# Optimization experiments

Measured on AMD Instinct MI355X. Metric: run time of the kernel, lower is better.

The kernel has to match this reference:

```python
import jax, jax.numpy as jnp
import numpy as np

N = 100000
NNZ = 3200000
F = 128


def setup_inputs() -> dict:
    key = jax.random.key(0)
    k1, k2, k3 = jax.random.split(key, 3)
    x = jax.random.normal(k1, (N, F), dtype=jnp.float32)
    A_ind = jax.random.randint(k2, (2, NNZ), 0, N, dtype=jnp.int64)
    A_val = jax.random.normal(k3, (NNZ,), dtype=jnp.float32)
    return {"x": x, "A_ind": A_ind, "A_val": A_val}


def reference(x, A_ind, A_val):
    # COO SpMM: out[r] = sum over edges e with row[e]==r of A_val[e] * x[col[e]]
    # coalesce() in torch sums duplicate (row, col) entries; segment_sum over
    # rows yields identical math without explicit sorting/deduplication.
    row, col = A_ind[0], A_ind[1]
    contrib = A_val[:, None] * x[col]            # [nnz, F] gather + scale
    out = jax.ops.segment_sum(contrib, row, num_segments=x.shape[0])  # scatter-add
    return out
```

## Files before the change

### kernel.cpp

```cpp
#include <hip/hip_runtime.h>

#define F 128
#define RPB 64
#define MAXNB 1792
#define CHUNK 8192
#define EPT 32
#define CAP 3072
#define SPMM_T 512
#define HELD (CAP/SPMM_T)

__global__ void spmm_coo_atomic(const int* __restrict__ rows,
                                const int* __restrict__ cols,
                                const float* __restrict__ vals,
                                const float* __restrict__ x,
                                float* __restrict__ out,
                                int nnz, int n_rows) {
    int t = blockIdx.x * blockDim.x + threadIdx.x;
    int e = t >> 5;
    int g = t & 31;
    if (e >= nnz) return;
    int r = rows[e];
    int c = cols[e];
    float v = vals[e];
    if ((unsigned)r >= (unsigned)n_rows || (unsigned)c >= (unsigned)n_rows) return;
    const float4 xv = *reinterpret_cast<const float4*>(x + (size_t)c * F + g * 4);
    float* o = out + (size_t)r * F + g * 4;
    atomicAdd(o + 0, v * xv.x);
    atomicAdd(o + 1, v * xv.y);
    atomicAdd(o + 2, v * xv.z);
    atomicAdd(o + 3, v * xv.w);
}

__device__ __forceinline__ unsigned f2bf(float f) {
    unsigned u = __float_as_uint(f);
    return (u + 0x7FFFu + ((u >> 16) & 1u)) >> 16;
}

__global__ void k_cvt_bf16(const float* __restrict__ x, unsigned short* __restrict__ xb,
                           long long total) {
    long long i = ((long long)blockIdx.x * 256 + threadIdx.x) * 8;
    if (i >= total) return;
    float4 a = *reinterpret_cast<const float4*>(x + i);
    float4 b = *reinterpret_cast<const float4*>(x + i + 4);
    uint4 o;
    o.x = f2bf(a.x) | (f2bf(a.y) << 16);
    o.y = f2bf(a.z) | (f2bf(a.w) << 16);
    o.z = f2bf(b.x) | (f2bf(b.y) << 16);
    o.w = f2bf(b.z) | (f2bf(b.w) << 16);
    *reinterpret_cast<uint4*>(xb + i) = o;
}

__global__ void k_bucket_histo(const int* __restrict__ rows, int* __restrict__ cnt,
                               int nnz, int nbk, int n) {
    __shared__ int lc[MAXNB];
    for (int i = threadIdx.x; i < nbk; i += 256) lc[i] = 0;
    __syncthreads();
    int base = blockIdx.x * CHUNK;
#pragma unroll
    for (int k = 0; k < EPT; ++k) {
        int e = base + k * 256 + threadIdx.x;
        if (e < nnz) {
            int r = rows[e];
            if ((unsigned)r < (unsigned)n) atomicAdd(&lc[r / RPB], 1);
        }
    }
    __syncthreads();
    for (int i = threadIdx.x; i < nbk; i += 256) {
        int c = lc[i];
        if (c) atomicAdd(&cnt[i], c);
    }
}

__global__ void k_bucket_scan(const int* __restrict__ cnt, int* __restrict__ off,
                              int* __restrict__ gcur, int nbk) {
    __shared__ int s[256];
    int tid = threadIdx.x;
    int per = (nbk + 255) / 256;
    int base = tid * per;
    int loc[8];
    int tsum = 0;
#pragma unroll
    for (int k = 0; k < 8; ++k) {
        int i = base + k;
        int v = (k < per && i < nbk) ? cnt[i] : 0;
        loc[k] = v;
        tsum += v;
    }
    s[tid] = tsum;
    __syncthreads();
    for (int o = 1; o < 256; o <<= 1) {
        int t = (tid >= o) ? s[tid - o] : 0;
        __syncthreads();
        s[tid] += t;
        __syncthreads();
    }
    int run = s[tid] - tsum;
#pragma unroll
    for (int k = 0; k < 8; ++k) {
        int i = base + k;
        if (k < per && i < nbk) { off[i] = run; gcur[i] = run; }
        run += loc[k];
    }
    if (tid == 255) off[nbk] = s[255];
}

__global__ void k_rank_scatter(const int* __restrict__ rows, const int* __restrict__ cols,
                               const float* __restrict__ vals, int* __restrict__ gcur,
                               int2* __restrict__ pair, int nnz, int nbk, int n) {
    __shared__ int lcnt[MAXNB];
    __shared__ int lbase[MAXNB];
    for (int i = threadIdx.x; i < nbk; i += 256) lcnt[i] = 0;
    __syncthreads();
    int base = blockIdx.x * CHUNK;
    unsigned br[EPT];
#pragma unroll
    for (int k = 0; k < EPT; ++k) {
        int e = base + k * 256 + threadIdx.x;
        br[k] = 0xFFFFFFFFu;
        if (e < nnz) {
            int r = rows[e];
            if ((unsigned)r < (unsigned)n) {
                int b = r / RPB;
                int rk = atomicAdd(&lcnt[b], 1);
                br[k] = ((unsigned)b << 13) | (unsigned)rk;
            }
        }
    }
    __syncthreads();
    for (int i = threadIdx.x; i < nbk; i += 256) {
        int c = lcnt[i];
        if (c) lbase[i] = atomicAdd(&gcur[i], c);
    }
    __syncthreads();
#pragma unroll
    for (int k = 0; k < EPT; ++k) {
        if (br[k] != 0xFFFFFFFFu) {
            int e = base + k * 256 + threadIdx.x;
            int b = br[k] >> 13;
            int rk = br[k] & 0x1FFF;
            int lr = rows[e] - b * RPB;
            int c = cols[e];
            if ((unsigned)c >= (unsigned)n) c = 0;
            int pos = lbase[b] + rk;
            pair[pos] = make_int2((lr << 17) | c, __float_as_int(vals[e]));
        }
    }
}

__global__ void __launch_bounds__(SPMM_T) k_sort_spmm(const int* __restrict__ off,
                                                      const int2* __restrict__ pair,
                                                      const unsigned short* __restrict__ xb,
                                                      float* __restrict__ out, int n) {
    __shared__ int2 eb[CAP];
    __shared__ int rcnt[RPB];
    __shared__ int rst[RPB + 1];
    __shared__ int rcur[RPB];

    int b = blockIdx.x;
    int tid = threadIdx.x;
    int wave = tid >> 6;
    int lane = tid & 63;
    int q = lane >> 4;
    int fl = lane & 15;

    int beg = off[b], end = off[b + 1];
    bool first = true;
    int bb = beg;
    do {
        int bn = min(CAP, end - bb);
        if (tid < RPB) rcnt[tid] = 0;
        __syncthreads();

        int2 held[HELD];
#pragma unroll
        for (int k = 0; k < HELD; ++k) {
            int j = tid + k * SPMM_T;
            held[k] = make_int2(0, 0);
            if (j < bn) {
                int2 pr = pair[bb + j];
                held[k] = pr;
                atomicAdd(&rcnt[pr.x >> 17], 1);
            }
        }
        __syncthreads();

        if (tid < 64) {
            int v = rcnt[tid];
            int s = v;
            for (int o = 1; o < 64; o <<= 1) {
                int t = __shfl_up(s, o);
                if (tid >= o) s += t;
            }
            rst[tid + 1] = s;
            if (tid == 0) rst[0] = 0;
            rcur[tid] = s - v;
        }
        __syncthreads();

#pragma unroll
        for (int k = 0; k < HELD; ++k) {
            int j = tid + k * SPMM_T;
            if (j < bn) {
                int2 pr = held[k];
                int lr = pr.x >> 17;
                int pos = atomicAdd(&rcur[lr], 1);
                eb[pos] = make_int2(pr.x & 0x1FFFF, pr.y);
            }
        }
        __syncthreads();

        for (int rr = 0; rr < 8; ++rr) {
            int lr = wave * 8 + rr;
            int s0 = rst[lr], s1 = rst[lr + 1];
            float acc[8] = {0.f, 0.f, 0.f, 0.f, 0.f, 0.f, 0.f, 0.f};
#pragma unroll 2
            for (int j = s0 + q; j < s1; j += 4) {
                int2 e = eb[j];
                int col = e.x;
                float vk = __int_as_float(e.y);
                uint4 w = *reinterpret_cast<const uint4*>(xb + (size_t)col * F + fl * 8);
                acc[0] += vk * __uint_as_float(w.x << 16);
                acc[1] += vk * __uint_as_float(w.x & 0xFFFF0000u);
                acc[2] += vk * __uint_as_float(w.y << 16);
                acc[3] += vk * __uint_as_float(w.y & 0xFFFF0000u);
                acc[4] += vk * __uint_as_float(w.z << 16);
                acc[5] += vk * __uint_as_float(w.z & 0xFFFF0000u);
                acc[6] += vk * __uint_as_float(w.w << 16);
                acc[7] += vk * __uint_as_float(w.w & 0xFFFF0000u);
            }
#pragma unroll
            for (int i = 0; i < 8; ++i) {
                acc[i] += __shfl_xor(acc[i], 16);
                acc[i] += __shfl_xor(acc[i], 32);
            }
            if (q == 0) {
                long long row = (long long)b * RPB + lr;
                if (row < n) {
                    float* po = out + (size_t)row * F + fl * 8;
                    float4 lo = make_float4(acc[0], acc[1], acc[2], acc[3]);
                    float4 hi = make_float4(acc[4], acc[5], acc[6], acc[7]);
                    if (first) {
                        *reinterpret_cast<float4*>(po) = lo;
                        *reinterpret_cast<float4*>(po + 4) = hi;
                    } else {
                        float4 t0 = *reinterpret_cast<const float4*>(po);
                        float4 t1 = *reinterpret_cast<const float4*>(po + 4);
                        t0.x += lo.x; t0.y += lo.y; t0.z += lo.z; t0.w += lo.w;
                        t1.x += hi.x; t1.y += hi.y; t1.z += hi.z; t1.w += hi.w;
                        *reinterpret_cast<float4*>(po) = t0;
                        *reinterpret_cast<float4*>(po + 4) = t1;
                    }
                }
            }
        }
        first = false;
        bb += CAP;
        __syncthreads();
    } while (bb < end);
}

extern "C" void kernel_launch(void* const* d_in, const int* in_sizes, int n_in,
                              void* d_out, int out_size, void* d_ws, size_t ws_size,
                              hipStream_t stream) {
    const float* x = (const float*)d_in[0];
    const int* A_ind = (const int*)d_in[1];
    const float* A_val = (const float*)d_in[2];
    float* out = (float*)d_out;

    const int nnz = in_sizes[2];
    const int n = out_size / F;
    const int nbk = (n + RPB - 1) / RPB;
    const int* rows = A_ind;
    const int* cols = A_ind + nnz;

    const long long xtotal = (long long)n * F;

    const size_t need = (size_t)nnz * 8
                      + (size_t)xtotal * 2
                      + (size_t)(3 * nbk + 1) * 4 + 128;

    if (nbk > MAXNB || (xtotal % 8) != 0 || ws_size < need) {
        hipMemsetAsync(d_out, 0, (size_t)out_size * sizeof(float), stream);
        const long long total = (long long)nnz * 32;
        spmm_coo_atomic<<<(int)((total + 255) / 256), 256, 0, stream>>>(
            rows, cols, A_val, x, out, nnz, n);
        return;
    }

    char* w = (char*)d_ws;
    int2* pair = (int2*)w;            w += (size_t)nnz * 8;
    unsigned short* xb = (unsigned short*)w;  w += (size_t)xtotal * 2;
    int* cnt = (int*)w;               w += (size_t)nbk * 4;
    int* off = (int*)w;               w += (size_t)(nbk + 1) * 4;
    int* gcur = (int*)w;

    const int nchunks = (nnz + CHUNK - 1) / CHUNK;

    k_cvt_bf16<<<(int)(xtotal / 8 + 255) / 256, 256, 0, stream>>>(x, xb, xtotal);
    hipMemsetAsync(cnt, 0, (size_t)nbk * 4, stream);
    k_bucket_histo<<<nchunks, 256, 0, stream>>>(rows, cnt, nnz, nbk, n);
    k_bucket_scan<<<1, 256, 0, stream>>>(cnt, off, gcur, nbk);
    k_rank_scatter<<<nchunks, 256, 0, stream>>>(rows, cols, A_val, gcur, pair,
                                                nnz, nbk, n);
    k_sort_spmm<<<nbk, SPMM_T, 0, stream>>>(off, pair, xb, out, n);
}
```

Baseline: 223.5 us.

## Fuse bf16 conversion with histogram and make SpMM kernel persistent

Merges the x-to-bf16 conversion kernel and the bucket histogram kernel into a single launch, splitting blocks by index, so one launch is saved and the two independent jobs can overlap. The sort-SpMM kernel becomes a grid-stride persistent kernel capped at 1024 blocks instead of one block per bucket. With ~1563 buckets, some blocks now process two buckets serially, which may cause load imbalance at the tail.

```diff
diff --git a/kernel.cpp b/kernel.cpp
--- a/kernel.cpp
+++ b/kernel.cpp
@@ -8,6 +8,7 @@
 #define CAP 3072
 #define SPMM_T 512
 #define HELD (CAP/SPMM_T)
+#define PERSIST 1024
 
 __global__ void spmm_coo_atomic(const int* __restrict__ rows,
                                 const int* __restrict__ cols,
@@ -36,38 +37,39 @@
     return (u + 0x7FFFu + ((u >> 16) & 1u)) >> 16;
 }
 
-__global__ void k_cvt_bf16(const float* __restrict__ x, unsigned short* __restrict__ xb,
-                           long long total) {
-    long long i = ((long long)blockIdx.x * 256 + threadIdx.x) * 8;
-    if (i >= total) return;
-    float4 a = *reinterpret_cast<const float4*>(x + i);
-    float4 b = *reinterpret_cast<const float4*>(x + i + 4);
-    uint4 o;
-    o.x = f2bf(a.x) | (f2bf(a.y) << 16);
-    o.y = f2bf(a.z) | (f2bf(a.w) << 16);
-    o.z = f2bf(b.x) | (f2bf(b.y) << 16);
-    o.w = f2bf(b.z) | (f2bf(b.w) << 16);
-    *reinterpret_cast<uint4*>(xb + i) = o;
-}
-
-__global__ void k_bucket_histo(const int* __restrict__ rows, int* __restrict__ cnt,
-                               int nnz, int nbk, int n) {
+__global__ void k_cvt_histo(const float* __restrict__ x, unsigned short* __restrict__ xb,
+                            long long xtotal,
+                            const int* __restrict__ rows, int* __restrict__ cnt,
+                            int nnz, int nbk, int n, int cvtb) {
     __shared__ int lc[MAXNB];
-    for (int i = threadIdx.x; i < nbk; i += 256) lc[i] = 0;
-    __syncthreads();
-    int base = blockIdx.x * CHUNK;
-#pragma unroll
-    for (int k = 0; k < EPT; ++k) {
-        int e = base + k * 256 + threadIdx.x;
-        if (e < nnz) {
-            int r = rows[e];
-            if ((unsigned)r < (unsigned)n) atomicAdd(&lc[r / RPB], 1);
+    if ((int)blockIdx.x < cvtb) {
+        long long i = ((long long)blockIdx.x * 256 + threadIdx.x) * 8;
+        if (i >= xtotal) return;
+        float4 a = *reinterpret_cast<const float4*>(x + i);
+        float4 b = *reinterpret_cast<const float4*>(x + i + 4);
+        uint4 o;
+        o.x = f2bf(a.x) | (f2bf(a.y) << 16);
+        o.y = f2bf(a.z) | (f2bf(a.w) << 16);
+        o.z = f2bf(b.x) | (f2bf(b.y) << 16);
+        o.w = f2bf(b.z) | (f2bf(b.w) << 16);
+        *reinterpret_cast<uint4*>(xb + i) = o;
+    } else {
+        for (int i = threadIdx.x; i < nbk; i += 256) lc[i] = 0;
+        __syncthreads();
+        int base = ((int)blockIdx.x - cvtb) * CHUNK;
+#pragma unroll
+        for (int k = 0; k < EPT; ++k) {
+            int e = base + k * 256 + threadIdx.x;
+            if (e < nnz) {
+                int r = rows[e];
+                if ((unsigned)r < (unsigned)n) atomicAdd(&lc[r / RPB], 1);
+            }
         }
-    }
-    __syncthreads();
-    for (int i = threadIdx.x; i < nbk; i += 256) {
-        int c = lc[i];
-        if (c) atomicAdd(&cnt[i], c);
+        __syncthreads();
+        for (int i = threadIdx.x; i < nbk; i += 256) {
+            int c = lc[i];
+            if (c) atomicAdd(&cnt[i], c);
+        }
     }
 }
 
@@ -150,113 +152,115 @@
 __global__ void __launch_bounds__(SPMM_T) k_sort_spmm(const int* __restrict__ off,
                                                       const int2* __restrict__ pair,
                                                       const unsigned short* __restrict__ xb,
-                                                      float* __restrict__ out, int n) {
+                                                      float* __restrict__ out,
+                                                      int n, int nbk) {
     __shared__ int2 eb[CAP];
     __shared__ int rcnt[RPB];
     __shared__ int rst[RPB + 1];
     __shared__ int rcur[RPB];
 
-    int b = blockIdx.x;
     int tid = threadIdx.x;
     int wave = tid >> 6;
     int lane = tid & 63;
     int q = lane >> 4;
     int fl = lane & 15;
 
-    int beg = off[b], end = off[b + 1];
-    bool first = true;
-    int bb = beg;
-    do {
-        int bn = min(CAP, end - bb);
-        if (tid < RPB) rcnt[tid] = 0;
-        __syncthreads();
-
-        int2 held[HELD];
-#pragma unroll
-        for (int k = 0; k < HELD; ++k) {
-            int j = tid + k * SPMM_T;
-            held[k] = make_int2(0, 0);
-            if (j < bn) {
-                int2 pr = pair[bb + j];
-                held[k] = pr;
-                atomicAdd(&rcnt[pr.x >> 17], 1);
-            }
-        }
-        __syncthreads();
-
-        if (tid < 64) {
-            int v = rcnt[tid];
-            int s = v;
-            for (int o = 1; o < 64; o <<= 1) {
-                int t = __shfl_up(s, o);
-                if (tid >= o) s += t;
-            }
-            rst[tid + 1] = s;
-            if (tid == 0) rst[0] = 0;
-            rcur[tid] = s - v;
-        }
-        __syncthreads();
-
-#pragma unroll
-        for (int k = 0; k < HELD; ++k) {
-            int j = tid + k * SPMM_T;
-            if (j < bn) {
-                int2 pr = held[k];
-                int lr = pr.x >> 17;
-                int pos = atomicAdd(&rcur[lr], 1);
-                eb[pos] = make_int2(pr.x & 0x1FFFF, pr.y);
-            }
-        }
-        __syncthreads();
-
-        for (int rr = 0; rr < 8; ++rr) {
-            int lr = wave * 8 + rr;
-            int s0 = rst[lr], s1 = rst[lr + 1];
-            float acc[8] = {0.f, 0.f, 0.f, 0.f, 0.f, 0.f, 0.f, 0.f};
+    for (int b = blockIdx.x; b < nbk; b += gridDim.x) {
+        int beg = off[b], end = off[b + 1];
+        bool first = true;
+        int bb = beg;
+        do {
+            int bn = min(CAP, end - bb);
+            if (tid < RPB) rcnt[tid] = 0;
+            __syncthreads();
+
+            int2 held[HELD];
+#pragma unroll
+            for (int k = 0; k < HELD; ++k) {
+                int j = tid + k * SPMM_T;
+                held[k] = make_int2(0, 0);
+                if (j < bn) {
+                    int2 pr = pair[bb + j];
+                    held[k] = pr;
+                    atomicAdd(&rcnt[pr.x >> 17], 1);
+                }
+            }
+            __syncthreads();
+
+            if (tid < RPB) {
+                int v = rcnt[tid];
+                int s = v;
+                for (int o = 1; o < RPB; o <<= 1) {
+                    int t = __shfl_up(s, o);
+                    if (tid >= o) s += t;
+                }
+                rst[tid + 1] = s;
+                if (tid == 0) rst[0] = 0;
+                rcur[tid] = s - v;
+            }
+            __syncthreads();
+
+#pragma unroll
+            for (int k = 0; k < HELD; ++k) {
+                int j = tid + k * SPMM_T;
+                if (j < bn) {
+                    int2 pr = held[k];
+                    int lr = pr.x >> 17;
+                    int pos = atomicAdd(&rcur[lr], 1);
+                    eb[pos] = make_int2(pr.x & 0x1FFFF, pr.y);
+                }
+            }
+            __syncthreads();
+
+            for (int rr = 0; rr < 8; ++rr) {
+                int lr = wave * 8 + rr;
+                int s0 = rst[lr], s1 = rst[lr + 1];
+                float acc[8] = {0.f, 0.f, 0.f, 0.f, 0.f, 0.f, 0.f, 0.f};
 #pragma unroll 2
-            for (int j = s0 + q; j < s1; j += 4) {
-                int2 e = eb[j];
-                int col = e.x;
-                float vk = __int_as_float(e.y);
-                uint4 w = *reinterpret_cast<const uint4*>(xb + (size_t)col * F + fl * 8);
-                acc[0] += vk * __uint_as_float(w.x << 16);
-                acc[1] += vk * __uint_as_float(w.x & 0xFFFF0000u);
-                acc[2] += vk * __uint_as_float(w.y << 16);
-                acc[3] += vk * __uint_as_float(w.y & 0xFFFF0000u);
-                acc[4] += vk * __uint_as_float(w.z << 16);
-                acc[5] += vk * __uint_as_float(w.z & 0xFFFF0000u);
-                acc[6] += vk * __uint_as_float(w.w << 16);
-                acc[7] += vk * __uint_as_float(w.w & 0xFFFF0000u);
-            }
-#pragma unroll
-            for (int i = 0; i < 8; ++i) {
-                acc[i] += __shfl_xor(acc[i], 16);
-                acc[i] += __shfl_xor(acc[i], 32);
-            }
-            if (q == 0) {
-                long long row = (long long)b * RPB + lr;
-                if (row < n) {
-                    float* po = out + (size_t)row * F + fl * 8;
-                    float4 lo = make_float4(acc[0], acc[1], acc[2], acc[3]);
-                    float4 hi = make_float4(acc[4], acc[5], acc[6], acc[7]);
-                    if (first) {
-                        *reinterpret_cast<float4*>(po) = lo;
-                        *reinterpret_cast<float4*>(po + 4) = hi;
-                    } else {
-                        float4 t0 = *reinterpret_cast<const float4*>(po);
-                        float4 t1 = *reinterpret_cast<const float4*>(po + 4);
-                        t0.x += lo.x; t0.y += lo.y; t0.z += lo.z; t0.w += lo.w;
-                        t1.x += hi.x; t1.y += hi.y; t1.z += hi.z; t1.w += hi.w;
-                        *reinterpret_cast<float4*>(po) = t0;
-                        *reinterpret_cast<float4*>(po + 4) = t1;
+                for (int j = s0 + q; j < s1; j += 4) {
+                    int2 e = eb[j];
+                    int col = e.x;
+                    float vk = __int_as_float(e.y);
+                    uint4 w = *reinterpret_cast<const uint4*>(xb + (size_t)col * F + fl * 8);
+                    acc[0] += vk * __uint_as_float(w.x << 16);
+                    acc[1] += vk * __uint_as_float(w.x & 0xFFFF0000u);
+                    acc[2] += vk * __uint_as_float(w.y << 16);
+                    acc[3] += vk * __uint_as_float(w.y & 0xFFFF0000u);
+                    acc[4] += vk * __uint_as_float(w.z << 16);
+                    acc[5] += vk * __uint_as_float(w.z & 0xFFFF0000u);
+                    acc[6] += vk * __uint_as_float(w.w << 16);
+                    acc[7] += vk * __uint_as_float(w.w & 0xFFFF0000u);
+                }
+#pragma unroll
+                for (int i = 0; i < 8; ++i) {
+                    acc[i] += __shfl_xor(acc[i], 16);
+                    acc[i] += __shfl_xor(acc[i], 32);
+                }
+                if (q == 0) {
+                    long long row = (long long)b * RPB + lr;
+                    if (row < n) {
+                        float* po = out + (size_t)row * F + fl * 8;
+                        float4 lo = make_float4(acc[0], acc[1], acc[2], acc[3]);
+                        float4 hi = make_float4(acc[4], acc[5], acc[6], acc[7]);
+                        if (first) {
+                            *reinterpret_cast<float4*>(po) = lo;
+                            *reinterpret_cast<float4*>(po + 4) = hi;
+                        } else {
+                            float4 t0 = *reinterpret_cast<const float4*>(po);
+                            float4 t1 = *reinterpret_cast<const float4*>(po + 4);
+                            t0.x += lo.x; t0.y += lo.y; t0.z += lo.z; t0.w += lo.w;
+                            t1.x += hi.x; t1.y += hi.y; t1.z += hi.z; t1.w += hi.w;
+                            *reinterpret_cast<float4*>(po) = t0;
+                            *reinterpret_cast<float4*>(po + 4) = t1;
+                        }
                     }
                 }
             }
-        }
-        first = false;
-        bb += CAP;
-        __syncthreads();
-    } while (bb < end);
+            first = false;
+            bb += CAP;
+            __syncthreads();
+        } while (bb < end);
+    }
 }
 
 extern "C" void kernel_launch(void* const* d_in, const int* in_sizes, int n_in,
@@ -295,12 +299,14 @@
     int* gcur = (int*)w;
 
     const int nchunks = (nnz + CHUNK - 1) / CHUNK;
-
-    k_cvt_bf16<<<(int)(xtotal / 8 + 255) / 256, 256, 0, stream>>>(x, xb, xtotal);
+    const int cvtb = (int)((xtotal / 8 + 255) / 256);
+
     hipMemsetAsync(cnt, 0, (size_t)nbk * 4, stream);
-    k_bucket_histo<<<nchunks, 256, 0, stream>>>(rows, cnt, nnz, nbk, n);
+    k_cvt_histo<<<cvtb + nchunks, 256, 0, stream>>>(x, xb, xtotal, rows, cnt,
+                                                    nnz, nbk, n, cvtb);
     k_bucket_scan<<<1, 256, 0, stream>>>(cnt, off, gcur, nbk);
     k_rank_scatter<<<nchunks, 256, 0, stream>>>(rows, cols, A_val, gcur, pair,
                                                 nnz, nbk, n);
-    k_sort_spmm<<<nbk, SPMM_T, 0, stream>>>(off, pair, xb, out, n);
-}
+    const int pgrid = (nbk < PERSIST) ? nbk : PERSIST;
+    k_sort_spmm<<<pgrid, SPMM_T, 0, stream>>>(off, pair, xb, out, n, nbk);
+}
```

New measurement: 216.7 us. 1.03x faster.
